# Kernel optimization log

Measured on AMD Instinct MI355X. Metric: run time of the kernel, lower is better.

## Reference

```python
import jax, jax.numpy as jnp
import numpy as np

B, T, C = 4, 2048, 1024
H = 16
D = C // H  # head_dim = 64


def setup_inputs() -> dict:
    key = jax.random.key(0)
    ks = jax.random.split(key, 9)
    s = 1.0 / np.sqrt(C)
    return {
        "x": jax.random.normal(ks[0], (B, T, C), dtype=jnp.float32),
        "Wk": jax.random.uniform(ks[1], (C, C), jnp.float32, -s, s),
        "bk": jax.random.uniform(ks[2], (C,), jnp.float32, -s, s),
        "Wq": jax.random.uniform(ks[3], (C, C), jnp.float32, -s, s),
        "bq": jax.random.uniform(ks[4], (C,), jnp.float32, -s, s),
        "Wv": jax.random.uniform(ks[5], (C, C), jnp.float32, -s, s),
        "bv": jax.random.uniform(ks[6], (C,), jnp.float32, -s, s),
        "Wp": jax.random.uniform(ks[7], (C, C), jnp.float32, -s, s),
        "bp": jax.random.uniform(ks[8], (C,), jnp.float32, -s, s),
    }


def reference(x, Wk, bk, Wq, bq, Wv, bv, Wp, bp):
    # projections -> (B, H, T, D)
    def split_heads(y):
        return y.reshape(B, T, H, D).transpose(0, 2, 1, 3)

    k = split_heads(x @ Wk.T + bk)
    q = split_heads(x @ Wq.T + bq)
    v = split_heads(x @ Wv.T + bv)

    att = jnp.einsum("bhtd,bhsd->bhts", q, k) / np.sqrt(D).astype(np.float32)
    causal = jnp.tril(jnp.ones((T, T), dtype=bool))
    att = jnp.where(causal, att, -jnp.inf)
    att = jax.nn.softmax(att, axis=-1)

    y = jnp.einsum("bhts,bhsd->bhtd", att, v)  # (B,H,T,D)
    y = y.transpose(0, 2, 1, 3).reshape(B, T, C)
    return y @ Wp.T + bp
```

## Files before the change

kernel.cpp:

```cpp
#include <hip/hip_runtime.h>
#include <hip/hip_bf16.h>

typedef unsigned short u16;
typedef unsigned int u32;
typedef short short8 __attribute__((ext_vector_type(8)));
typedef short short4v __attribute__((ext_vector_type(4)));
typedef float f32x4 __attribute__((ext_vector_type(4)));

#define MFMA16(a, b, c) __builtin_amdgcn_mfma_f32_16x16x32_bf16((a), (b), (c), 0, 0, 0)

constexpr int kB = 4, kT = 2048, kC = 1024, kH = 16, kD = 64;
constexpr int kBT = kB * kT;
constexpr long kQKV = (long)kB * kH * kT * kD;
constexpr float kSC = 0.125f * 1.4426950408889634f;

__device__ inline u16 f2bf(float f) {
    __hip_bfloat16 h = __float2bfloat16(f);
    return *reinterpret_cast<u16*>(&h);
}
__device__ inline u32 pkbf_trunc(float lo, float hi) {
    return __builtin_amdgcn_perm(__builtin_bit_cast(u32, hi),
                                 __builtin_bit_cast(u32, lo), 0x07060302u);
}
__device__ inline u32 pkbf_rne(float lo, float hi) {
    return ((u32)f2bf(hi) << 16) | (u32)f2bf(lo);
}

__device__ inline void cp16(const u16* g, u16* l) {
    __builtin_amdgcn_global_load_lds(
        (const __attribute__((address_space(1))) unsigned int*)g,
        (__attribute__((address_space(3))) unsigned int*)l, 16, 0, 0);
}

__global__ __launch_bounds__(256) void cast_kernel(
    const float* __restrict__ x,  const float* __restrict__ Wk,
    const float* __restrict__ Wq, const float* __restrict__ Wv,
    const float* __restrict__ Wp,
    u16* __restrict__ xb, u16* __restrict__ wkb, u16* __restrict__ wqb,
    u16* __restrict__ wvb, u16* __restrict__ wpb)
{
    const long id = (long)blockIdx.x * 256 + threadIdx.x;
    const float* src;
    u16* dst;
    long off;
    if (id < 2097152) {
        src = x; dst = xb; off = id;
    } else {
        const long w = (id - 2097152) >> 18;
        off = (id - 2097152) & 262143;
        src = (w == 0) ? Wk : (w == 1) ? Wq : (w == 2) ? Wv : Wp;
        dst = (w == 0) ? wkb : (w == 1) ? wqb : (w == 2) ? wvb : wpb;
    }
    f32x4 v = *(const f32x4*)&src[off * 4];
    short4v s = {(short)f2bf(v[0]), (short)f2bf(v[1]),
                 (short)f2bf(v[2]), (short)f2bf(v[3])};
    *(short4v*)&dst[off * 4] = s;
}

__global__ __launch_bounds__(512, 1) void qkv_gemm_bf16(
    const u16* __restrict__ xb,
    const u16* __restrict__ wkb, const u16* __restrict__ wqb,
    const u16* __restrict__ wvb,
    const float* __restrict__ bk, const float* __restrict__ bq,
    const float* __restrict__ bv,
    u16* __restrict__ kw, u16* __restrict__ qw, u16* __restrict__ vw)
{
    __shared__ u16 A2[2][128 * 64];
    __shared__ u16 B2[2][256 * 64];

    const int tid = threadIdx.x;
    const int lane = tid & 63;
    const int wid = tid >> 6;
    const int l15 = lane & 15;
    const int quad = lane >> 4;
    const int wr = wid & 1;
    const int wc = wid >> 1;
    const int m0 = blockIdx.x * 128;
    const int n0 = blockIdx.y * 256;
    const int z = blockIdx.z;

    const u16* W = (z == 0) ? wkb : (z == 1) ? wqb : wvb;
    const float* bias = (z == 0) ? bk : (z == 1) ? bq : bv;

    f32x4 zero = {0.f, 0.f, 0.f, 0.f};
    f32x4 acc[4][4];
#pragma unroll
    for (int i = 0; i < 4; ++i)
#pragma unroll
        for (int j = 0; j < 4; ++j) acc[i][j] = zero;

    const u16* aSrc[2]; int aDst[2];
#pragma unroll
    for (int q = 0; q < 2; ++q) {
        const int slot = q * 512 + tid;
        const int row = slot >> 3, c = slot & 7;
        aSrc[q] = xb + (long)(m0 + row) * kC + ((c ^ (row & 7)) * 8);
        aDst[q] = slot * 8;
    }
    const u16* bSrc[4]; int bDst[4];
#pragma unroll
    for (int q = 0; q < 4; ++q) {
        const int slot = q * 512 + tid;
        const int row = slot >> 3, c = slot & 7;
        bSrc[q] = W + (long)(n0 + row) * kC + ((c ^ (row & 7)) * 8);
        bDst[q] = slot * 8;
    }

    auto stage = [&](int t, int cbuf) {
        const long ko = (long)t * 64;
#pragma unroll
        for (int q = 0; q < 2; ++q) cp16(aSrc[q] + ko, &A2[cbuf][aDst[q]]);
#pragma unroll
        for (int q = 0; q < 4; ++q) cp16(bSrc[q] + ko, &B2[cbuf][bDst[q]]);
    };

    int aOff[4][2], bOff[4][2];
#pragma unroll
    for (int mt = 0; mt < 4; ++mt) {
        const int row = wr * 64 + mt * 16 + l15;
#pragma unroll
        for (int k2 = 0; k2 < 2; ++k2)
            aOff[mt][k2] = row * 64 + (((k2 * 4 + quad) ^ (row & 7)) * 8);
    }
#pragma unroll
    for (int nt = 0; nt < 4; ++nt) {
        const int row = wc * 64 + nt * 16 + l15;
#pragma unroll
        for (int k2 = 0; k2 < 2; ++k2)
            bOff[nt][k2] = row * 64 + (((k2 * 4 + quad) ^ (row & 7)) * 8);
    }

    stage(0, 0);
    stage(1, 1);
    asm volatile("s_waitcnt vmcnt(6)" ::: "memory");
    __builtin_amdgcn_s_barrier();

    for (int t = 0; t < 16; ++t) {
        const int c = t & 1;
        short8 af[4][2], bf[4][2];
#pragma unroll
        for (int mt = 0; mt < 4; ++mt)
#pragma unroll
            for (int k2 = 0; k2 < 2; ++k2)
                af[mt][k2] = *(const short8*)&A2[c][aOff[mt][k2]];
#pragma unroll
        for (int nt = 0; nt < 4; ++nt)
#pragma unroll
            for (int k2 = 0; k2 < 2; ++k2)
                bf[nt][k2] = *(const short8*)&B2[c][bOff[nt][k2]];

        __builtin_amdgcn_s_setprio(1);
#pragma unroll
        for (int mt = 0; mt < 4; ++mt)
#pragma unroll
            for (int nt = 0; nt < 2; ++nt) {
                acc[mt][nt] = MFMA16(af[mt][0], bf[nt][0], acc[mt][nt]);
                acc[mt][nt] = MFMA16(af[mt][1], bf[nt][1], acc[mt][nt]);
            }
        __builtin_amdgcn_s_setprio(0);

        asm volatile("s_waitcnt lgkmcnt(0)" ::: "memory");
        __builtin_amdgcn_s_barrier();

        if (t + 2 < 16) stage(t + 2, c);

        __builtin_amdgcn_s_setprio(1);
#pragma unroll
        for (int mt = 0; mt < 4; ++mt)
#pragma unroll
            for (int nt = 2; nt < 4; ++nt) {
                acc[mt][nt] = MFMA16(af[mt][0], bf[nt][0], acc[mt][nt]);
                acc[mt][nt] = MFMA16(af[mt][1], bf[nt][1], acc[mt][nt]);
            }
        __builtin_amdgcn_s_setprio(0);

        if (t + 2 < 16) {
            asm volatile("s_waitcnt vmcnt(6)" ::: "memory");
        } else {
            asm volatile("s_waitcnt vmcnt(0)" ::: "memory");
        }
        __builtin_amdgcn_s_barrier();
    }

    const float scale = (z == 1) ? kSC : 1.0f;
#pragma unroll
    for (int nt = 0; nt < 4; ++nt) {
        const int n = n0 + wc * 64 + nt * 16 + l15;
        const float bias_f = bias[n];
        const int h = n >> 6, d = n & 63;
#pragma unroll
        for (int mt = 0; mt < 4; ++mt) {
#pragma unroll
            for (int r = 0; r < 4; ++r) {
                const int m = m0 + wr * 64 + mt * 16 + quad * 4 + r;
                const int b = m >> 11, t = m & 2047;
                const float v = (acc[mt][nt][r] + bias_f) * scale;
                const int bh = b * kH + h;
                if (z == 2) {
                    vw[((long)bh * kD + d) * kT + t] = f2bf(v);
                } else {
                    u16* dst = (z == 0) ? kw : qw;
                    dst[((long)bh * kT + t) * kD + d] = f2bf(v);
                }
            }
        }
    }
}

__global__ __launch_bounds__(256) void qkv_gemm_kernel(
    const float* __restrict__ x,
    const float* __restrict__ Wk, const float* __restrict__ bk,
    const float* __restrict__ Wq, const float* __restrict__ bq,
    const float* __restrict__ Wv, const float* __restrict__ bv,
    u16* __restrict__ kw, u16* __restrict__ qw, u16* __restrict__ vw)
{
    __shared__ u16 As[128 * 32];
    __shared__ u16 Bs[128 * 32];
    const int tid = threadIdx.x;
    const int lane = tid & 63;
    const int wid = tid >> 6;
    const int l15 = lane & 15;
    const int quad = lane >> 4;
    const int m0 = blockIdx.x * 128;
    const int n0 = blockIdx.y * 128;
    const int z = blockIdx.z;

    const float* W = (z == 0) ? Wk : (z == 1) ? Wq : Wv;
    const float* bias = (z == 0) ? bk : (z == 1) ? bq : bv;

    f32x4 zero = {0.f, 0.f, 0.f, 0.f};
    f32x4 acc[4][4];
#pragma unroll
    for (int i = 0; i < 4; ++i)
#pragma unroll
        for (int j = 0; j < 4; ++j) acc[i][j] = zero;

    const int wm = (wid & 1) * 64;
    const int wn = (wid >> 1) * 64;
    const int row4 = tid >> 3;
    const int col4 = (tid & 7) * 4;

    for (int k0 = 0; k0 < kC; k0 += 32) {
#pragma unroll
        for (int p = 0; p < 4; ++p) {
            const int r = p * 32 + row4;
            f32x4 xa = *(const f32x4*)&x[(long)(m0 + r) * kC + k0 + col4];
            f32x4 wa = *(const f32x4*)&W[(long)(n0 + r) * kC + k0 + col4];
            short4v xs = {(short)f2bf(xa[0]), (short)f2bf(xa[1]),
                          (short)f2bf(xa[2]), (short)f2bf(xa[3])};
            short4v wsv = {(short)f2bf(wa[0]), (short)f2bf(wa[1]),
                           (short)f2bf(wa[2]), (short)f2bf(wa[3])};
            *(short4v*)&As[r * 32 + col4] = xs;
            *(short4v*)&Bs[r * 32 + col4] = wsv;
        }
        __syncthreads();
        short8 af[4], bfr[4];
#pragma unroll
        for (int mt = 0; mt < 4; ++mt)
            af[mt] = *(const short8*)&As[(wm + mt * 16 + l15) * 32 + quad * 8];
#pragma unroll
        for (int nt = 0; nt < 4; ++nt)
            bfr[nt] = *(const short8*)&Bs[(wn + nt * 16 + l15) * 32 + quad * 8];
#pragma unroll
        for (int mt = 0; mt < 4; ++mt)
#pragma unroll
            for (int nt = 0; nt < 4; ++nt)
                acc[mt][nt] = MFMA16(af[mt], bfr[nt], acc[mt][nt]);
        __syncthreads();
    }

    const float scale = (z == 1) ? kSC : 1.0f;
#pragma unroll
    for (int nt = 0; nt < 4; ++nt) {
        const int n = n0 + wn + nt * 16 + l15;
        const float bias_f = bias[n];
        const int h = n >> 6, d = n & 63;
#pragma unroll
        for (int mt = 0; mt < 4; ++mt) {
#pragma unroll
            for (int r = 0; r < 4; ++r) {
                const int m = m0 + wm + mt * 16 + quad * 4 + r;
                const int b = m >> 11, t = m & 2047;
                const float v = (acc[mt][nt][r] + bias_f) * scale;
                const int bh = b * kH + h;
                if (z == 2) {
                    vw[((long)bh * kD + d) * kT + t] = f2bf(v);
                } else {
                    u16* dst = (z == 0) ? kw : qw;
                    dst[((long)bh * kT + t) * kD + d] = f2bf(v);
                }
            }
        }
    }
}

__global__ __launch_bounds__(128, 2) void attn_kernel(
    const u16* qw, const u16* kw, const u16* vw, u16* ow)
{
    __shared__ u16 Ks[2][64 * 64];
    __shared__ u16 VT[2][64 * 64];
    __shared__ u16 Pb[64 * 64];

    const int tid = threadIdx.x;
    const int lane = tid & 63;
    const int wid = tid >> 6;
    const int l15 = lane & 15;
    const int quad = lane >> 4;
    const int id = blockIdx.x;
    const int bh = id & 63;
    const int pr = id >> 6;

    const float NEG = -1.0e30f;
    f32x4 zero = {0.f, 0.f, 0.f, 0.f};
    const short8 onesf = {(short)0x3F80, (short)0x3F80, (short)0x3F80, (short)0x3F80,
                          (short)0x3F80, (short)0x3F80, (short)0x3F80, (short)0x3F80};

    const int rl7 = l15 & 7;

    const u16* kbase = kw + (long)bh * kT * kD;
    const u16* vbase = vw + (long)bh * kD * kT;

    const u16* kp[4];
    const u16* vp[4];
#pragma unroll
    for (int q = 0; q < 4; ++q) {
        const int slot = q * 128 + tid;
        const int row = slot >> 3;
        const int c = slot & 7;
        const int off = (c ^ (row & 7)) * 8;
        kp[q] = kbase + (long)row * kD + off;
        vp[q] = vbase + (long)row * kT + off;
    }

    auto stage = [&](int buf, int st) {
        u16* kd = Ks[buf];
        u16* vd = VT[buf];
#pragma unroll
        for (int q = 0; q < 4; ++q) {
            cp16(kp[q] + (long)st * (64 * kD), kd + (q * 128 + tid) * 8);
            cp16(vp[q] + st * 64,              vd + (q * 128 + tid) * 8);
        }
    };

#pragma unroll
    for (int ph = 0; ph < 2; ++ph) {
        const int qt64 = ph ? (31 - pr) : pr;
        const int tw = qt64 * 64 + wid * 32;
        const int n_st = qt64 + 1;

        __syncthreads();
        stage(0, 0);

        short8 qf[2][2];
#pragma unroll
        for (int g = 0; g < 2; ++g) {
            const u16* qp = qw + ((long)bh * kT + tw + g * 16 + l15) * kD;
            qf[g][0] = *(const short8*)&qp[quad * 8];
            qf[g][1] = *(const short8*)&qp[32 + quad * 8];
        }

        f32x4 oacc[4][2];
#pragma unroll
        for (int mo = 0; mo < 4; ++mo)
#pragma unroll
            for (int g = 0; g < 2; ++g) oacc[mo][g] = zero;
        f32x4 lsum[2] = {zero, zero};

        for (int st = 0; st < n_st; ++st) {
            __syncthreads();
            const int cur = st & 1;
            if (st + 1 < n_st) stage(cur ^ 1, st + 1);

            const u16* K_ = Ks[cur];
            const u16* V_ = VT[cur];

            f32x4 sacc[4][2];
            __builtin_amdgcn_s_setprio(1);
#pragma unroll
            for (int ms = 0; ms < 4; ++ms) {
                const int row = ms * 16 + l15;
                short8 kf0 = *(const short8*)&K_[row * 64 + ((quad ^ rl7) * 8)];
                short8 kf1 = *(const short8*)&K_[row * 64 + (((4 + quad) ^ rl7) * 8)];
#pragma unroll
                for (int g = 0; g < 2; ++g) {
                    sacc[ms][g] = MFMA16(kf0, qf[g][0], zero);
                    sacc[ms][g] = MFMA16(kf1, qf[g][1], sacc[ms][g]);
                }
            }
            __builtin_amdgcn_s_setprio(0);

            if (st == n_st - 1) {
#pragma unroll
                for (int g = 0; g < 2; ++g) {
                    const int tl = wid * 32 + g * 16 + l15;
#pragma unroll
                    for (int ms = 0; ms < 4; ++ms)
#pragma unroll
                        for (int r = 0; r < 4; ++r)
                            if (ms * 16 + quad * 4 + r > tl) sacc[ms][g][r] = NEG;
                }
            }

#pragma unroll
            for (int g = 0; g < 2; ++g) {
                const int prow = wid * 32 + g * 16 + l15;
#pragma unroll
                for (int ms = 0; ms < 4; ++ms) {
                    const float p0 = exp2f(sacc[ms][g][0]);
                    const float p1 = exp2f(sacc[ms][g][1]);
                    const float p2 = exp2f(sacc[ms][g][2]);
                    const float p3 = exp2f(sacc[ms][g][3]);
                    uint2 pk;
                    pk.x = pkbf_trunc(p0, p1);
                    pk.y = pkbf_trunc(p2, p3);
                    const int chunk = (ms * 2 + (quad >> 1)) ^ rl7;
                    *(uint2*)&Pb[prow * 64 + chunk * 8 + (quad & 1) * 4] = pk;
                }
            }

            short8 pf[2][2];
#pragma unroll
            for (int g = 0; g < 2; ++g) {
                const int prow = wid * 32 + g * 16 + l15;
                pf[g][0] = *(const short8*)&Pb[prow * 64 + ((quad ^ rl7) * 8)];
                pf[g][1] = *(const short8*)&Pb[prow * 64 + (((4 + quad) ^ rl7) * 8)];
                lsum[g] = MFMA16(onesf, pf[g][0], lsum[g]);
                lsum[g] = MFMA16(onesf, pf[g][1], lsum[g]);
            }

            __builtin_amdgcn_s_setprio(1);
#pragma unroll
            for (int mo = 0; mo < 4; ++mo) {
                const int row = mo * 16 + l15;
                short8 vf0 = *(const short8*)&V_[row * 64 + ((quad ^ rl7) * 8)];
                short8 vf1 = *(const short8*)&V_[row * 64 + (((4 + quad) ^ rl7) * 8)];
#pragma unroll
                for (int g = 0; g < 2; ++g) {
                    oacc[mo][g] = MFMA16(vf0, pf[g][0], oacc[mo][g]);
                    oacc[mo][g] = MFMA16(vf1, pf[g][1], oacc[mo][g]);
                }
            }
            __builtin_amdgcn_s_setprio(0);
        }

#pragma unroll
        for (int g = 0; g < 2; ++g) {
            const float inv = 1.0f / lsum[g][0];
            const int t = tw + g * 16 + l15;
            u16* op = ow + ((long)bh * kT + t) * kD;
#pragma unroll
            for (int mo = 0; mo < 4; ++mo) {
                uint2 ov;
                ov.x = pkbf_rne(oacc[mo][g][0] * inv, oacc[mo][g][1] * inv);
                ov.y = pkbf_rne(oacc[mo][g][2] * inv, oacc[mo][g][3] * inv);
                *(uint2*)&op[mo * 16 + quad * 4] = ov;
            }
        }
    }
}

__global__ __launch_bounds__(512, 1) void out_gemm_bf16(
    const u16* __restrict__ ob, const u16* __restrict__ wpb,
    const float* __restrict__ bp, float* __restrict__ out)
{
    __shared__ u16 A2[2][128 * 64];
    __shared__ u16 B2[2][256 * 64];

    const int tid = threadIdx.x;
    const int lane = tid & 63;
    const int wid = tid >> 6;
    const int l15 = lane & 15;
    const int quad = lane >> 4;
    const int wr = wid & 1;
    const int wc = wid >> 1;
    const int m0 = blockIdx.x * 128;
    const int n0 = blockIdx.y * 256;

    f32x4 zero = {0.f, 0.f, 0.f, 0.f};
    f32x4 acc[4][4];
#pragma unroll
    for (int i = 0; i < 4; ++i)
#pragma unroll
        for (int j = 0; j < 4; ++j) acc[i][j] = zero;

    const u16* aSrc[2]; int aDst[2];
#pragma unroll
    for (int q = 0; q < 2; ++q) {
        const int slot = q * 512 + tid;
        const int row = slot >> 3, c = slot & 7;
        const int m = m0 + row, b = m >> 11, trow = m & 2047;
        aSrc[q] = ob + (((long)b * kH) * kT + trow) * kD + ((c ^ (row & 7)) * 8);
        aDst[q] = slot * 8;
    }
    const u16* bSrc[4]; int bDst[4];
#pragma unroll
    for (int q = 0; q < 4; ++q) {
        const int slot = q * 512 + tid;
        const int row = slot >> 3, c = slot & 7;
        bSrc[q] = wpb + (long)(n0 + row) * kC + ((c ^ (row & 7)) * 8);
        bDst[q] = slot * 8;
    }

    auto stage = [&](int t, int cbuf) {
        const long koA = (long)t * kT * kD;
        const long koB = (long)t * 64;
#pragma unroll
        for (int q = 0; q < 2; ++q) cp16(aSrc[q] + koA, &A2[cbuf][aDst[q]]);
#pragma unroll
        for (int q = 0; q < 4; ++q) cp16(bSrc[q] + koB, &B2[cbuf][bDst[q]]);
    };

    int aOff[4][2], bOff[4][2];
#pragma unroll
    for (int mt = 0; mt < 4; ++mt) {
        const int row = wr * 64 + mt * 16 + l15;
#pragma unroll
        for (int k2 = 0; k2 < 2; ++k2)
            aOff[mt][k2] = row * 64 + (((k2 * 4 + quad) ^ (row & 7)) * 8);
    }
#pragma unroll
    for (int nt = 0; nt < 4; ++nt) {
        const int row = wc * 64 + nt * 16 + l15;
#pragma unroll
        for (int k2 = 0; k2 < 2; ++k2)
            bOff[nt][k2] = row * 64 + (((k2 * 4 + quad) ^ (row & 7)) * 8);
    }

    stage(0, 0);
    stage(1, 1);
    asm volatile("s_waitcnt vmcnt(6)" ::: "memory");
    __builtin_amdgcn_s_barrier();

    for (int t = 0; t < 16; ++t) {
        const int c = t & 1;
        short8 af[4][2], bf[4][2];
#pragma unroll
        for (int mt = 0; mt < 4; ++mt)
#pragma unroll
            for (int k2 = 0; k2 < 2; ++k2)
                af[mt][k2] = *(const short8*)&A2[c][aOff[mt][k2]];
#pragma unroll
        for (int nt = 0; nt < 4; ++nt)
#pragma unroll
            for (int k2 = 0; k2 < 2; ++k2)
                bf[nt][k2] = *(const short8*)&B2[c][bOff[nt][k2]];

        __builtin_amdgcn_s_setprio(1);
#pragma unroll
        for (int mt = 0; mt < 4; ++mt)
#pragma unroll
            for (int nt = 0; nt < 2; ++nt) {
                acc[mt][nt] = MFMA16(af[mt][0], bf[nt][0], acc[mt][nt]);
                acc[mt][nt] = MFMA16(af[mt][1], bf[nt][1], acc[mt][nt]);
            }
        __builtin_amdgcn_s_setprio(0);

        asm volatile("s_waitcnt lgkmcnt(0)" ::: "memory");
        __builtin_amdgcn_s_barrier();

        if (t + 2 < 16) stage(t + 2, c);

        __builtin_amdgcn_s_setprio(1);
#pragma unroll
        for (int mt = 0; mt < 4; ++mt)
#pragma unroll
            for (int nt = 2; nt < 4; ++nt) {
                acc[mt][nt] = MFMA16(af[mt][0], bf[nt][0], acc[mt][nt]);
                acc[mt][nt] = MFMA16(af[mt][1], bf[nt][1], acc[mt][nt]);
            }
        __builtin_amdgcn_s_setprio(0);

        if (t + 2 < 16) {
            asm volatile("s_waitcnt vmcnt(6)" ::: "memory");
        } else {
            asm volatile("s_waitcnt vmcnt(0)" ::: "memory");
        }
        __builtin_amdgcn_s_barrier();
    }

#pragma unroll
    for (int nt = 0; nt < 4; ++nt) {
        const int n = n0 + wc * 64 + nt * 16 + l15;
        const float bias_f = bp[n];
#pragma unroll
        for (int mt = 0; mt < 4; ++mt) {
#pragma unroll
            for (int r = 0; r < 4; ++r) {
                const int m = m0 + wr * 64 + mt * 16 + quad * 4 + r;
                out[(long)m * kC + n] = acc[mt][nt][r] + bias_f;
            }
        }
    }
}

__global__ __launch_bounds__(256) void out_gemm_kernel(
    const u16* __restrict__ ow, const float* __restrict__ Wp,
    const float* __restrict__ bp, float* __restrict__ out)
{
    __shared__ u16 As[128 * 32];
    __shared__ u16 Bs[128 * 32];
    const int tid = threadIdx.x;
    const int lane = tid & 63;
    const int wid = tid >> 6;
    const int l15 = lane & 15;
    const int quad = lane >> 4;
    const int m0 = blockIdx.x * 128;
    const int n0 = blockIdx.y * 128;

    f32x4 zero = {0.f, 0.f, 0.f, 0.f};
    f32x4 acc[4][4];
#pragma unroll
    for (int i = 0; i < 4; ++i)
#pragma unroll
        for (int j = 0; j < 4; ++j) acc[i][j] = zero;

    const int wm = (wid & 1) * 64;
    const int wn = (wid >> 1) * 64;

    const int r0 = tid >> 2;
    const int kkA = (tid & 3) * 8;
    const int r1 = r0 + 64;
    const int row4 = tid >> 3;
    const int col4 = (tid & 7) * 4;

    for (int k0 = 0; k0 < kC; k0 += 32) {
        {
            const int m = m0 + r0, b = m >> 11, t = m & 2047;
            const int kk = k0 + kkA, h = kk >> 6, d = kk & 63;
            *(short8*)&As[r0 * 32 + kkA] =
                *(const short8*)&ow[(((long)b * kH + h) * kT + t) * kD + d];
        }
        {
            const int m = m0 + r1, b = m >> 11, t = m & 2047;
            const int kk = k0 + kkA, h = kk >> 6, d = kk & 63;
            *(short8*)&As[r1 * 32 + kkA] =
                *(const short8*)&ow[(((long)b * kH + h) * kT + t) * kD + d];
        }
#pragma unroll
        for (int p = 0; p < 4; ++p) {
            const int r = p * 32 + row4;
            f32x4 wa = *(const f32x4*)&Wp[(long)(n0 + r) * kC + k0 + col4];
            short4v wsv = {(short)f2bf(wa[0]), (short)f2bf(wa[1]),
                           (short)f2bf(wa[2]), (short)f2bf(wa[3])};
            *(short4v*)&Bs[r * 32 + col4] = wsv;
        }
        __syncthreads();
        short8 af[4], bfr[4];
#pragma unroll
        for (int mt = 0; mt < 4; ++mt)
            af[mt] = *(const short8*)&As[(wm + mt * 16 + l15) * 32 + quad * 8];
#pragma unroll
        for (int nt = 0; nt < 4; ++nt)
            bfr[nt] = *(const short8*)&Bs[(wn + nt * 16 + l15) * 32 + quad * 8];
#pragma unroll
        for (int mt = 0; mt < 4; ++mt)
#pragma unroll
            for (int nt = 0; nt < 4; ++nt)
                acc[mt][nt] = MFMA16(af[mt], bfr[nt], acc[mt][nt]);
        __syncthreads();
    }

#pragma unroll
    for (int nt = 0; nt < 4; ++nt) {
        const int n = n0 + wn + nt * 16 + l15;
        const float bias_f = bp[n];
#pragma unroll
        for (int mt = 0; mt < 4; ++mt) {
#pragma unroll
            for (int r = 0; r < 4; ++r) {
                const int m = m0 + wm + mt * 16 + quad * 4 + r;
                out[(long)m * kC + n] = acc[mt][nt][r] + bias_f;
            }
        }
    }
}

extern "C" void kernel_launch(void* const* d_in, const int* in_sizes, int n_in,
                              void* d_out, int out_size, void* d_ws, size_t ws_size,
                              hipStream_t stream) {
    const float* x  = (const float*)d_in[0];
    const float* Wk = (const float*)d_in[1];
    const float* bk = (const float*)d_in[2];
    const float* Wq = (const float*)d_in[3];
    const float* bq = (const float*)d_in[4];
    const float* Wv = (const float*)d_in[5];
    const float* bv = (const float*)d_in[6];
    const float* Wp = (const float*)d_in[7];
    const float* bp = (const float*)d_in[8];
    float* out = (float*)d_out;

    u16* ws = (u16*)d_ws;
    const size_t kNeed = 72ull * 1024 * 1024;

    if (ws_size >= kNeed) {
        u16* k_ws = ws;
        u16* q_ws = ws + kQKV;
        u16* v_ws = ws + 2 * kQKV;
        u16* xb   = ws + 3 * kQKV;
        u16* o_ws = xb;
        u16* wkb  = ws + 4 * kQKV;
        u16* wqb  = wkb + (long)kC * kC;
        u16* wvb  = wqb + (long)kC * kC;
        u16* wpb  = wvb + (long)kC * kC;

        cast_kernel<<<12288, 256, 0, stream>>>(x, Wk, Wq, Wv, Wp,
                                               xb, wkb, wqb, wvb, wpb);
        qkv_gemm_bf16<<<dim3(kBT / 128, kC / 256, 3), 512, 0, stream>>>(
            xb, wkb, wqb, wvb, bk, bq, bv, k_ws, q_ws, v_ws);
        attn_kernel<<<1024, 128, 0, stream>>>(q_ws, k_ws, v_ws, o_ws);
        out_gemm_bf16<<<dim3(kBT / 128, kC / 256), 512, 0, stream>>>(
            o_ws, wpb, bp, out);
    } else {
        u16* k_ws = ws;
        u16* q_ws = ws + kQKV;
        u16* v_ws = ws + 2 * kQKV;
        u16* o_ws = q_ws;

        qkv_gemm_kernel<<<dim3(kBT / 128, kC / 128, 3), 256, 0, stream>>>(
            x, Wk, bk, Wq, bq, Wv, bv, k_ws, q_ws, v_ws);
        attn_kernel<<<1024, 128, 0, stream>>>(q_ws, k_ws, v_ws, o_ws);
        out_gemm_kernel<<<dim3(kBT / 128, kC / 128), 256, 0, stream>>>(
            o_ws, Wp, bp, out);
    }
}
```

Measured before the change: 266.8 us.

## Interleave split-phase global prefetch with quadrant MFMA blocks in bf16 GEMMs

Result: faster. 257.0 us (-3.7%).

```diff
diff --git a/kernel.cpp b/kernel.cpp
--- a/kernel.cpp
+++ b/kernel.cpp
@@ -57,16 +57,15 @@
     *(short4v*)&dst[off * 4] = s;
 }
 
+
 __global__ __launch_bounds__(512, 1) void qkv_gemm_bf16(
-    const u16* __restrict__ xb,
-    const u16* __restrict__ wkb, const u16* __restrict__ wqb,
-    const u16* __restrict__ wvb,
+    const u16* __restrict__ xb, const u16* __restrict__ wall,
     const float* __restrict__ bk, const float* __restrict__ bq,
     const float* __restrict__ bv,
     u16* __restrict__ kw, u16* __restrict__ qw, u16* __restrict__ vw)
 {
-    __shared__ u16 A2[2][128 * 64];
-    __shared__ u16 B2[2][256 * 64];
+    __shared__ __align__(16) u16 A2[2][128 * 64];
+    __shared__ __align__(16) u16 B2[2][256 * 64];
 
     const int tid = threadIdx.x;
     const int lane = tid & 63;
@@ -76,11 +75,7 @@
     const int wr = wid & 1;
     const int wc = wid >> 1;
     const int m0 = blockIdx.x * 128;
-    const int n0 = blockIdx.y * 256;
-    const int z = blockIdx.z;
-
-    const u16* W = (z == 0) ? wkb : (z == 1) ? wqb : wvb;
-    const float* bias = (z == 0) ? bk : (z == 1) ? bq : bv;
+    const int n0c = blockIdx.y * 256;
 
     f32x4 zero = {0.f, 0.f, 0.f, 0.f};
     f32x4 acc[4][4];
@@ -89,118 +84,173 @@
 #pragma unroll
         for (int j = 0; j < 4; ++j) acc[i][j] = zero;
 
-    const u16* aSrc[2]; int aDst[2];
+    const int vA = tid >> 3, chA = tid & 7;
+    const int rowMa = ((vA >> 5) << 6) + (vA & 31);
+    const int rowMb = rowMa + 32;
+    const u16* aMaS = xb + (long)(m0 + rowMa) * kC + ((chA ^ (rowMa & 7)) * 8);
+    const u16* aMbS = xb + (long)(m0 + rowMb) * kC + ((chA ^ (rowMb & 7)) * 8);
+    const int aMaD = rowMa * 64 + chA * 8;
+    const int aMbD = rowMb * 64 + chA * 8;
+    const u16* bNaS[2]; const u16* bNbS[2];
+    int bNaD[2], bNbD[2];
 #pragma unroll
     for (int q = 0; q < 2; ++q) {
         const int slot = q * 512 + tid;
-        const int row = slot >> 3, c = slot & 7;
-        aSrc[q] = xb + (long)(m0 + row) * kC + ((c ^ (row & 7)) * 8);
-        aDst[q] = slot * 8;
-    }
-    const u16* bSrc[4]; int bDst[4];
-#pragma unroll
-    for (int q = 0; q < 4; ++q) {
-        const int slot = q * 512 + tid;
-        const int row = slot >> 3, c = slot & 7;
-        bSrc[q] = W + (long)(n0 + row) * kC + ((c ^ (row & 7)) * 8);
-        bDst[q] = slot * 8;
-    }
-
-    auto stage = [&](int t, int cbuf) {
-        const long ko = (long)t * 64;
-#pragma unroll
-        for (int q = 0; q < 2; ++q) cp16(aSrc[q] + ko, &A2[cbuf][aDst[q]]);
-#pragma unroll
-        for (int q = 0; q < 4; ++q) cp16(bSrc[q] + ko, &B2[cbuf][bDst[q]]);
-    };
+        const int v = slot >> 3, ch = slot & 7;
+        const int ra = ((v >> 5) << 6) + (v & 31);
+        const int rb = ra + 32;
+        bNaS[q] = wall + (long)(n0c + ra) * kC + ((ch ^ (ra & 7)) * 8);
+        bNbS[q] = wall + (long)(n0c + rb) * kC + ((ch ^ (rb & 7)) * 8);
+        bNaD[q] = ra * 64 + ch * 8;
+        bNbD[q] = rb * 64 + ch * 8;
+    }
 
     int aOff[4][2], bOff[4][2];
 #pragma unroll
-    for (int mt = 0; mt < 4; ++mt) {
-        const int row = wr * 64 + mt * 16 + l15;
+    for (int i = 0; i < 4; ++i) {
+        const int row = wr * 64 + i * 16 + l15;
 #pragma unroll
         for (int k2 = 0; k2 < 2; ++k2)
-            aOff[mt][k2] = row * 64 + (((k2 * 4 + quad) ^ (row & 7)) * 8);
-    }
-#pragma unroll
-    for (int nt = 0; nt < 4; ++nt) {
-        const int row = wc * 64 + nt * 16 + l15;
+            aOff[i][k2] = row * 64 + (((k2 * 4 + quad) ^ (row & 7)) * 8);
+    }
+#pragma unroll
+    for (int j = 0; j < 4; ++j) {
+        const int row = wc * 64 + j * 16 + l15;
 #pragma unroll
         for (int k2 = 0; k2 < 2; ++k2)
-            bOff[nt][k2] = row * 64 + (((k2 * 4 + quad) ^ (row & 7)) * 8);
-    }
-
-    stage(0, 0);
-    stage(1, 1);
-    asm volatile("s_waitcnt vmcnt(6)" ::: "memory");
-    __builtin_amdgcn_s_barrier();
-
+            bOff[j][k2] = row * 64 + (((k2 * 4 + quad) ^ (row & 7)) * 8);
+    }
+
+    cp16(bNaS[0], &B2[0][bNaD[0]]);
+    cp16(bNaS[1], &B2[0][bNaD[1]]);
+    cp16(aMaS,    &A2[0][aMaD]);
+    cp16(aMbS,    &A2[0][aMbD]);
+    cp16(bNbS[0], &B2[0][bNbD[0]]);
+    cp16(bNbS[1], &B2[0][bNbD[1]]);
+
+#pragma unroll 2
     for (int t = 0; t < 16; ++t) {
         const int c = t & 1;
-        short8 af[4][2], bf[4][2];
-#pragma unroll
-        for (int mt = 0; mt < 4; ++mt)
+        const u16* Ab = A2[c];
+        const u16* Bb = B2[c];
+        u16* An = A2[c ^ 1];
+        u16* Bn = B2[c ^ 1];
+        const long ko = (long)(t + 1) * 64;
+        const bool pf = (t < 15);
+
+        short8 amL[2][2], amH[2][2], bnL[2][2], bnH[2][2];
+
+        asm volatile("s_waitcnt vmcnt(2)" ::: "memory");
+        __builtin_amdgcn_s_barrier();
+        __builtin_amdgcn_sched_barrier(0);
+#pragma unroll
+        for (int i = 0; i < 2; ++i)
 #pragma unroll
             for (int k2 = 0; k2 < 2; ++k2)
-                af[mt][k2] = *(const short8*)&A2[c][aOff[mt][k2]];
-#pragma unroll
-        for (int nt = 0; nt < 4; ++nt)
+                amL[i][k2] = *(const short8*)&Ab[aOff[i][k2]];
+#pragma unroll
+        for (int j = 0; j < 2; ++j)
 #pragma unroll
             for (int k2 = 0; k2 < 2; ++k2)
-                bf[nt][k2] = *(const short8*)&B2[c][bOff[nt][k2]];
-
+                bnL[j][k2] = *(const short8*)&Bb[bOff[j][k2]];
+        if (pf) {
+            cp16(bNaS[0] + ko, &Bn[bNaD[0]]);
+            cp16(bNaS[1] + ko, &Bn[bNaD[1]]);
+        }
+        asm volatile("s_waitcnt lgkmcnt(0)" ::: "memory");
+        __builtin_amdgcn_sched_barrier(0);
         __builtin_amdgcn_s_setprio(1);
 #pragma unroll
-        for (int mt = 0; mt < 4; ++mt)
-#pragma unroll
-            for (int nt = 0; nt < 2; ++nt) {
-                acc[mt][nt] = MFMA16(af[mt][0], bf[nt][0], acc[mt][nt]);
-                acc[mt][nt] = MFMA16(af[mt][1], bf[nt][1], acc[mt][nt]);
+        for (int i = 0; i < 2; ++i)
+#pragma unroll
+            for (int j = 0; j < 2; ++j) {
+                acc[i][j] = MFMA16(amL[i][0], bnL[j][0], acc[i][j]);
+                acc[i][j] = MFMA16(amL[i][1], bnL[j][1], acc[i][j]);
             }
         __builtin_amdgcn_s_setprio(0);
 
+#pragma unroll
+        for (int i = 0; i < 2; ++i)
+#pragma unroll
+            for (int k2 = 0; k2 < 2; ++k2)
+                amH[i][k2] = *(const short8*)&Ab[aOff[2 + i][k2]];
+        if (pf) {
+            cp16(aMaS + ko, &An[aMaD]);
+            cp16(aMbS + ko, &An[aMbD]);
+        }
         asm volatile("s_waitcnt lgkmcnt(0)" ::: "memory");
-        __builtin_amdgcn_s_barrier();
-
-        if (t + 2 < 16) stage(t + 2, c);
-
+        __builtin_amdgcn_sched_barrier(0);
         __builtin_amdgcn_s_setprio(1);
 #pragma unroll
-        for (int mt = 0; mt < 4; ++mt)
-#pragma unroll
-            for (int nt = 2; nt < 4; ++nt) {
-                acc[mt][nt] = MFMA16(af[mt][0], bf[nt][0], acc[mt][nt]);
-                acc[mt][nt] = MFMA16(af[mt][1], bf[nt][1], acc[mt][nt]);
+        for (int i = 0; i < 2; ++i)
+#pragma unroll
+            for (int j = 0; j < 2; ++j) {
+                acc[2 + i][j] = MFMA16(amH[i][0], bnL[j][0], acc[2 + i][j]);
+                acc[2 + i][j] = MFMA16(amH[i][1], bnL[j][1], acc[2 + i][j]);
             }
         __builtin_amdgcn_s_setprio(0);
 
-        if (t + 2 < 16) {
-            asm volatile("s_waitcnt vmcnt(6)" ::: "memory");
+        if (pf) {
+            asm volatile("s_waitcnt vmcnt(4)" ::: "memory");
         } else {
             asm volatile("s_waitcnt vmcnt(0)" ::: "memory");
         }
         __builtin_amdgcn_s_barrier();
-    }
-
+        __builtin_amdgcn_sched_barrier(0);
+#pragma unroll
+        for (int j = 0; j < 2; ++j)
+#pragma unroll
+            for (int k2 = 0; k2 < 2; ++k2)
+                bnH[j][k2] = *(const short8*)&Bb[bOff[2 + j][k2]];
+        if (pf) {
+            cp16(bNbS[0] + ko, &Bn[bNbD[0]]);
+            cp16(bNbS[1] + ko, &Bn[bNbD[1]]);
+        }
+        asm volatile("s_waitcnt lgkmcnt(0)" ::: "memory");
+        __builtin_amdgcn_sched_barrier(0);
+        __builtin_amdgcn_s_setprio(1);
+#pragma unroll
+        for (int i = 0; i < 2; ++i)
+#pragma unroll
+            for (int j = 0; j < 2; ++j) {
+                acc[i][2 + j] = MFMA16(amL[i][0], bnH[j][0], acc[i][2 + j]);
+                acc[i][2 + j] = MFMA16(amL[i][1], bnH[j][1], acc[i][2 + j]);
+            }
+        __builtin_amdgcn_s_setprio(0);
+
+        __builtin_amdgcn_s_setprio(1);
+#pragma unroll
+        for (int i = 0; i < 2; ++i)
+#pragma unroll
+            for (int j = 0; j < 2; ++j) {
+                acc[2 + i][2 + j] = MFMA16(amH[i][0], bnH[j][0], acc[2 + i][2 + j]);
+                acc[2 + i][2 + j] = MFMA16(amH[i][1], bnH[j][1], acc[2 + i][2 + j]);
+            }
+        __builtin_amdgcn_s_setprio(0);
+    }
+
+    const int z = (n0c >> 10);
     const float scale = (z == 1) ? kSC : 1.0f;
-#pragma unroll
-    for (int nt = 0; nt < 4; ++nt) {
-        const int n = n0 + wc * 64 + nt * 16 + l15;
-        const float bias_f = bias[n];
-        const int h = n >> 6, d = n & 63;
-#pragma unroll
-        for (int mt = 0; mt < 4; ++mt) {
+    const float* bias = (z == 0) ? bk : (z == 1) ? bq : bv;
+#pragma unroll
+    for (int j = 0; j < 4; ++j) {
+        const int n = n0c + wc * 64 + j * 16 + l15;
+        const int np = n & 1023;
+        const float bias_f = bias[np];
+        const int h = np >> 6, d = np & 63;
+#pragma unroll
+        for (int i = 0; i < 4; ++i) {
 #pragma unroll
             for (int r = 0; r < 4; ++r) {
-                const int m = m0 + wr * 64 + mt * 16 + quad * 4 + r;
-                const int b = m >> 11, t = m & 2047;
-                const float v = (acc[mt][nt][r] + bias_f) * scale;
+                const int m = m0 + wr * 64 + i * 16 + quad * 4 + r;
+                const int b = m >> 11, tt = m & 2047;
+                const float v = (acc[i][j][r] + bias_f) * scale;
                 const int bh = b * kH + h;
                 if (z == 2) {
-                    vw[((long)bh * kD + d) * kT + t] = f2bf(v);
+                    vw[((long)bh * kD + d) * kT + tt] = f2bf(v);
                 } else {
                     u16* dst = (z == 0) ? kw : qw;
-                    dst[((long)bh * kT + t) * kD + d] = f2bf(v);
+                    dst[((long)bh * kT + tt) * kD + d] = f2bf(v);
                 }
             }
         }
@@ -463,8 +513,8 @@
     const u16* __restrict__ ob, const u16* __restrict__ wpb,
     const float* __restrict__ bp, float* __restrict__ out)
 {
-    __shared__ u16 A2[2][128 * 64];
-    __shared__ u16 B2[2][256 * 64];
+    __shared__ __align__(16) u16 A2[2][128 * 64];
+    __shared__ __align__(16) u16 B2[2][256 * 64];
 
     const int tid = threadIdx.x;
     const int lane = tid & 63;
@@ -483,111 +533,166 @@
 #pragma unroll
         for (int j = 0; j < 4; ++j) acc[i][j] = zero;
 
-    const u16* aSrc[2]; int aDst[2];
+    const int vA = tid >> 3, chA = tid & 7;
+    const int rowMa = ((vA >> 5) << 6) + (vA & 31);
+    const int rowMb = rowMa + 32;
+    const int mMa = m0 + rowMa, mMb = m0 + rowMb;
+    const u16* aMaS = ob + (((long)(mMa >> 11) * kH) * kT + (mMa & 2047)) * kD
+                      + ((chA ^ (rowMa & 7)) * 8);
+    const u16* aMbS = ob + (((long)(mMb >> 11) * kH) * kT + (mMb & 2047)) * kD
+                      + ((chA ^ (rowMb & 7)) * 8);
+    const int aMaD = rowMa * 64 + chA * 8;
+    const int aMbD = rowMb * 64 + chA * 8;
+
+    const u16* bNaS[2]; const u16* bNbS[2];
+    int bNaD[2], bNbD[2];
 #pragma unroll
     for (int q = 0; q < 2; ++q) {
         const int slot = q * 512 + tid;
-        const int row = slot >> 3, c = slot & 7;
-        const int m = m0 + row, b = m >> 11, trow = m & 2047;
-        aSrc[q] = ob + (((long)b * kH) * kT + trow) * kD + ((c ^ (row & 7)) * 8);
-        aDst[q] = slot * 8;
-    }
-    const u16* bSrc[4]; int bDst[4];
-#pragma unroll
-    for (int q = 0; q < 4; ++q) {
-        const int slot = q * 512 + tid;
-        const int row = slot >> 3, c = slot & 7;
-        bSrc[q] = wpb + (long)(n0 + row) * kC + ((c ^ (row & 7)) * 8);
-        bDst[q] = slot * 8;
-    }
-
-    auto stage = [&](int t, int cbuf) {
-        const long koA = (long)t * kT * kD;
-        const long koB = (long)t * 64;
-#pragma unroll
-        for (int q = 0; q < 2; ++q) cp16(aSrc[q] + koA, &A2[cbuf][aDst[q]]);
-#pragma unroll
-        for (int q = 0; q < 4; ++q) cp16(bSrc[q] + koB, &B2[cbuf][bDst[q]]);
-    };
+        const int v = slot >> 3, ch = slot & 7;
+        const int ra = ((v >> 5) << 6) + (v & 31);
+        const int rb = ra + 32;
+        bNaS[q] = wpb + (long)(n0 + ra) * kC + ((ch ^ (ra & 7)) * 8);
+        bNbS[q] = wpb + (long)(n0 + rb) * kC + ((ch ^ (rb & 7)) * 8);
+        bNaD[q] = ra * 64 + ch * 8;
+        bNbD[q] = rb * 64 + ch * 8;
+    }
 
     int aOff[4][2], bOff[4][2];
 #pragma unroll
-    for (int mt = 0; mt < 4; ++mt) {
-        const int row = wr * 64 + mt * 16 + l15;
+    for (int i = 0; i < 4; ++i) {
+        const int row = wr * 64 + i * 16 + l15;
 #pragma unroll
         for (int k2 = 0; k2 < 2; ++k2)
-            aOff[mt][k2] = row * 64 + (((k2 * 4 + quad) ^ (row & 7)) * 8);
-    }
-#pragma unroll
-    for (int nt = 0; nt < 4; ++nt) {
-        const int row = wc * 64 + nt * 16 + l15;
+            aOff[i][k2] = row * 64 + (((k2 * 4 + quad) ^ (row & 7)) * 8);
+    }
+#pragma unroll
+    for (int j = 0; j < 4; ++j) {
+        const int row = wc * 64 + j * 16 + l15;
 #pragma unroll
         for (int k2 = 0; k2 < 2; ++k2)
-            bOff[nt][k2] = row * 64 + (((k2 * 4 + quad) ^ (row & 7)) * 8);
-    }
-
-    stage(0, 0);
-    stage(1, 1);
-    asm volatile("s_waitcnt vmcnt(6)" ::: "memory");
-    __builtin_amdgcn_s_barrier();
-
+            bOff[j][k2] = row * 64 + (((k2 * 4 + quad) ^ (row & 7)) * 8);
+    }
+
+    cp16(bNaS[0], &B2[0][bNaD[0]]);
+    cp16(bNaS[1], &B2[0][bNaD[1]]);
+    cp16(aMaS,    &A2[0][aMaD]);
+    cp16(aMbS,    &A2[0][aMbD]);
+    cp16(bNbS[0], &B2[0][bNbD[0]]);
+    cp16(bNbS[1], &B2[0][bNbD[1]]);
+
+#pragma unroll 2
     for (int t = 0; t < 16; ++t) {
         const int c = t & 1;
-        short8 af[4][2], bf[4][2];
-#pragma unroll
-        for (int mt = 0; mt < 4; ++mt)
+        const u16* Ab = A2[c];
+        const u16* Bb = B2[c];
+        u16* An = A2[c ^ 1];
+        u16* Bn = B2[c ^ 1];
+        const long koA = (long)(t + 1) * kT * kD;
+        const long koB = (long)(t + 1) * 64;
+        const bool pf = (t < 15);
+
+        short8 amL[2][2], amH[2][2], bnL[2][2], bnH[2][2];
+
+        asm volatile("s_waitcnt vmcnt(2)" ::: "memory");
+        __builtin_amdgcn_s_barrier();
+        __builtin_amdgcn_sched_barrier(0);
+#pragma unroll
+        for (int i = 0; i < 2; ++i)
 #pragma unroll
             for (int k2 = 0; k2 < 2; ++k2)
-                af[mt][k2] = *(const short8*)&A2[c][aOff[mt][k2]];
-#pragma unroll
-        for (int nt = 0; nt < 4; ++nt)
+                amL[i][k2] = *(const short8*)&Ab[aOff[i][k2]];
+#pragma unroll
+        for (int j = 0; j < 2; ++j)
 #pragma unroll
             for (int k2 = 0; k2 < 2; ++k2)
-                bf[nt][k2] = *(const short8*)&B2[c][bOff[nt][k2]];
-
+                bnL[j][k2] = *(const short8*)&Bb[bOff[j][k2]];
+        if (pf) {
+            cp16(bNaS[0] + koB, &Bn[bNaD[0]]);
+            cp16(bNaS[1] + koB, &Bn[bNaD[1]]);
+        }
+        asm volatile("s_waitcnt lgkmcnt(0)" ::: "memory");
+        __builtin_amdgcn_sched_barrier(0);
         __builtin_amdgcn_s_setprio(1);
 #pragma unroll
-        for (int mt = 0; mt < 4; ++mt)
-#pragma unroll
-            for (int nt = 0; nt < 2; ++nt) {
-                acc[mt][nt] = MFMA16(af[mt][0], bf[nt][0], acc[mt][nt]);
-                acc[mt][nt] = MFMA16(af[mt][1], bf[nt][1], acc[mt][nt]);
+        for (int i = 0; i < 2; ++i)
+#pragma unroll
+            for (int j = 0; j < 2; ++j) {
+                acc[i][j] = MFMA16(amL[i][0], bnL[j][0], acc[i][j]);
+                acc[i][j] = MFMA16(amL[i][1], bnL[j][1], acc[i][j]);
             }
         __builtin_amdgcn_s_setprio(0);
 
+#pragma unroll
+        for (int i = 0; i < 2; ++i)
+#pragma unroll
+            for (int k2 = 0; k2 < 2; ++k2)
+                amH[i][k2] = *(const short8*)&Ab[aOff[2 + i][k2]];
+        if (pf) {
+            cp16(aMaS + koA, &An[aMaD]);
+            cp16(aMbS + koA, &An[aMbD]);
+        }
         asm volatile("s_waitcnt lgkmcnt(0)" ::: "memory");
-        __builtin_amdgcn_s_barrier();
-
-        if (t + 2 < 16) stage(t + 2, c);
-
+        __builtin_amdgcn_sched_barrier(0);
         __builtin_amdgcn_s_setprio(1);
 #pragma unroll
-        for (int mt = 0; mt < 4; ++mt)
-#pragma unroll
-            for (int nt = 2; nt < 4; ++nt) {
-                acc[mt][nt] = MFMA16(af[mt][0], bf[nt][0], acc[mt][nt]);
-                acc[mt][nt] = MFMA16(af[mt][1], bf[nt][1], acc[mt][nt]);
+        for (int i = 0; i < 2; ++i)
+#pragma unroll
+            for (int j = 0; j < 2; ++j) {
+                acc[2 + i][j] = MFMA16(amH[i][0], bnL[j][0], acc[2 + i][j]);
+                acc[2 + i][j] = MFMA16(amH[i][1], bnL[j][1], acc[2 + i][j]);
             }
         __builtin_amdgcn_s_setprio(0);
 
-        if (t + 2 < 16) {
-            asm volatile("s_waitcnt vmcnt(6)" ::: "memory");
+        if (pf) {
+            asm volatile("s_waitcnt vmcnt(4)" ::: "memory");
         } else {
             asm volatile("s_waitcnt vmcnt(0)" ::: "memory");
         }
         __builtin_amdgcn_s_barrier();
-    }
-
-#pragma unroll
-    for (int nt = 0; nt < 4; ++nt) {
-        const int n = n0 + wc * 64 + nt * 16 + l15;
+        __builtin_amdgcn_sched_barrier(0);
+#pragma unroll
+        for (int j = 0; j < 2; ++j)
+#pragma unroll
+            for (int k2 = 0; k2 < 2; ++k2)
+                bnH[j][k2] = *(const short8*)&Bb[bOff[2 + j][k2]];
+        if (pf) {
+            cp16(bNbS[0] + koB, &Bn[bNbD[0]]);
+            cp16(bNbS[1] + koB, &Bn[bNbD[1]]);
+        }
+        asm volatile("s_waitcnt lgkmcnt(0)" ::: "memory");
+        __builtin_amdgcn_sched_barrier(0);
+        __builtin_amdgcn_s_setprio(1);
+#pragma unroll
+        for (int i = 0; i < 2; ++i)
+#pragma unroll
+            for (int j = 0; j < 2; ++j) {
+                acc[i][2 + j] = MFMA16(amL[i][0], bnH[j][0], acc[i][2 + j]);
+                acc[i][2 + j] = MFMA16(amL[i][1], bnH[j][1], acc[i][2 + j]);
+            }
+        __builtin_amdgcn_s_setprio(0);
+
+        __builtin_amdgcn_s_setprio(1);
+#pragma unroll
+        for (int i = 0; i < 2; ++i)
+#pragma unroll
+            for (int j = 0; j < 2; ++j) {
+                acc[2 + i][2 + j] = MFMA16(amH[i][0], bnH[j][0], acc[2 + i][2 + j]);
+                acc[2 + i][2 + j] = MFMA16(amH[i][1], bnH[j][1], acc[2 + i][2 + j]);
+            }
+        __builtin_amdgcn_s_setprio(0);
+    }
+
+#pragma unroll
+    for (int j = 0; j < 4; ++j) {
+        const int n = n0 + wc * 64 + j * 16 + l15;
         const float bias_f = bp[n];
 #pragma unroll
-        for (int mt = 0; mt < 4; ++mt) {
+        for (int i = 0; i < 4; ++i) {
 #pragma unroll
             for (int r = 0; r < 4; ++r) {
-                const int m = m0 + wr * 64 + mt * 16 + quad * 4 + r;
-                out[(long)m * kC + n] = acc[mt][nt][r] + bias_f;
+                const int m = m0 + wr * 64 + i * 16 + quad * 4 + r;
+                out[(long)m * kC + n] = acc[i][j][r] + bias_f;
             }
         }
     }
@@ -705,8 +810,8 @@
 
         cast_kernel<<<12288, 256, 0, stream>>>(x, Wk, Wq, Wv, Wp,
                                                xb, wkb, wqb, wvb, wpb);
-        qkv_gemm_bf16<<<dim3(kBT / 128, kC / 256, 3), 512, 0, stream>>>(
-            xb, wkb, wqb, wvb, bk, bq, bv, k_ws, q_ws, v_ws);
+        qkv_gemm_bf16<<<dim3(kBT / 128, 12), 512, 0, stream>>>(
+            xb, wkb, bk, bq, bv, k_ws, q_ws, v_ws);
         attn_kernel<<<1024, 128, 0, stream>>>(q_ws, k_ws, v_ws, o_ws);
         out_gemm_bf16<<<dim3(kBT / 128, kC / 256), 512, 0, stream>>>(
             o_ws, wpb, bp, out);
```
